# Performance work log

Measured on AMD Instinct MI355X. Metric: run time of the kernel, lower is better.

Reference implementation:

```python
import jax, jax.numpy as jnp
import numpy as np

N_DST = 25000
E = 400000
DN = 128   # dim_node
DE = 128   # dim_edge
DT = 128   # dim_time
DO = 128   # dim_out
H = 2      # num_head


def setup_inputs() -> dict:
    key = jax.random.key(0)
    ks = jax.random.split(key, 10)
    sc = 0.05
    node_h = jax.random.normal(ks[0], (N_DST + E, DN), jnp.float32)
    edge_f = jax.random.normal(ks[1], (E, DE), jnp.float32)
    dt = jax.random.uniform(ks[2], (E,), jnp.float32) * 100.0
    dst_idx = jax.random.randint(ks[3], (E,), 0, N_DST)
    # TimeEncode: Linear(1, dim_time) with w initialized to 1/10**linspace(0,9)
    time_w = jnp.asarray(1.0 / 10 ** np.linspace(0, 9, DT, dtype=np.float32))
    time_b = jnp.zeros((DT,), jnp.float32)
    Wq = jax.random.normal(ks[4], (DO, DN + DT), jnp.float32) * sc
    bq = jnp.zeros((DO,), jnp.float32)
    Wk = jax.random.normal(ks[5], (DO, DN + DE + DT), jnp.float32) * sc
    bk = jnp.zeros((DO,), jnp.float32)
    Wv = jax.random.normal(ks[6], (DO, DN + DE + DT), jnp.float32) * sc
    bv = jnp.zeros((DO,), jnp.float32)
    Wout = jax.random.normal(ks[7], (DO, DN + DO), jnp.float32) * sc
    bout = jnp.zeros((DO,), jnp.float32)
    gamma = jnp.ones((DO,), jnp.float32)
    beta = jnp.zeros((DO,), jnp.float32)
    return dict(node_h=node_h, edge_f=edge_f, dt=dt, dst_idx=dst_idx,
                time_w=time_w, time_b=time_b, Wq=Wq, bq=bq, Wk=Wk, bk=bk,
                Wv=Wv, bv=bv, Wout=Wout, bout=bout, gamma=gamma, beta=beta)


def reference(node_h, edge_f, dt, dst_idx, time_w, time_b,
              Wq, bq, Wk, bk, Wv, bv, Wout, bout, gamma, beta):
    num_dst = node_h.shape[0] - edge_f.shape[0]
    num_edges = edge_f.shape[0]
    tgt = node_h[:num_dst]            # [N, DN] target node embeddings
    src = node_h[num_dst:]            # [E, DN] per-edge source embeddings

    # TimeEncode: cos(w * dt + b)
    time_feats = jnp.cos(dt[:, None] * time_w[None, :] + time_b)          # [E, DT]
    zero_time = jnp.broadcast_to(jnp.cos(time_b), (num_dst, time_b.shape[0]))

    Qn = jnp.concatenate([tgt, zero_time], axis=1) @ Wq.T + bq            # [N, DO]
    kv_in = jnp.concatenate([src, edge_f, time_feats], axis=1)            # [E, DN+DE+DT]
    K = kv_in @ Wk.T + bk                                                 # [E, DO]
    V = kv_in @ Wv.T + bv                                                 # [E, DO]
    Q = Qn[dst_idx]                                                       # gather per edge

    d_head = Q.shape[1] // H
    Qh = Q.reshape(num_edges, H, d_head)
    Kh = K.reshape(num_edges, H, d_head)
    Vh = V.reshape(num_edges, H, d_head)

    score = jnp.sum(Qh * Kh, axis=2)                                      # [E, H]
    score = jnp.where(score >= 0, score, 0.2 * score)                     # LeakyReLU(0.2)

    # edge_softmax: segmented softmax over incoming edges of each dst node
    m = jax.ops.segment_max(score, dst_idx, num_segments=num_dst)
    m = jnp.where(jnp.isfinite(m), m, 0.0)                                # empty segments
    e = jnp.exp(score - m[dst_idx])
    s = jax.ops.segment_sum(e, dst_idx, num_segments=num_dst)
    att = e / s[dst_idx]                                                  # [E, H]

    Vw = (Vh * att[:, :, None]).reshape(num_edges, -1)                    # [E, DO]
    h = jax.ops.segment_sum(Vw, dst_idx, num_segments=num_dst)            # scatter-sum

    rst = jnp.concatenate([h, tgt], axis=1) @ Wout.T + bout               # [N, DO]
    rst = jax.nn.relu(rst)
    mu = jnp.mean(rst, axis=-1, keepdims=True)
    var = jnp.var(rst, axis=-1, keepdims=True)
    return (rst - mu) / jnp.sqrt(var + 1e-5) * gamma + beta
```

## Files before the change

kernel.cpp:

```cpp
#include <hip/hip_runtime.h>

#define N_DST 25000
#define E_NUM 400000

typedef __bf16 bf16x8 __attribute__((ext_vector_type(8)));
typedef __bf16 bf16x4 __attribute__((ext_vector_type(4)));
typedef __bf16 bf16x2 __attribute__((ext_vector_type(2)));
typedef float  f32x4  __attribute__((ext_vector_type(4)));

__device__ __forceinline__ float fast_cos(float x) {
  float r = x * 0.15915494309189535f;
  r = r - floorf(r);
  return __builtin_amdgcn_cosf(r);
}

__device__ __forceinline__ void pack_frag(const float* __restrict__ W0,
    const float* __restrict__ W1, int stride, int NC, int idx, __bf16* __restrict__ out) {
  int lane = idx & 63, fid = idx >> 6;
  int nfw = NC >> 6;
  int perks = nfw << 2;
  int ks = fid / perks, rem = fid - ks * perks;
  int w = rem / nfw, nf = rem - w * nfw;
  int n = w * (NC >> 2) + nf * 16 + (lane & 15);
  int g = (ks << 2) + (lane >> 4);
  const float* src = (W1 && n >= 128) ? (W1 + (size_t)(n - 128) * stride)
                                      : (W0 + (size_t)n * stride);
  const float4* s4 = reinterpret_cast<const float4*>(src + g * 8);
  float4 lo = s4[0], hi = s4[1];
  bf16x8 b;
  b[0]=(__bf16)lo.x; b[1]=(__bf16)lo.y; b[2]=(__bf16)lo.z; b[3]=(__bf16)lo.w;
  b[4]=(__bf16)hi.x; b[5]=(__bf16)hi.y; b[6]=(__bf16)hi.z; b[7]=(__bf16)hi.w;
  reinterpret_cast<bf16x8*>(out)[idx] = b;
}

__global__ __launch_bounds__(256) void prep_kernel(
    const float* __restrict__ Wq, const float* __restrict__ bq, const float* __restrict__ tb,
    const float* __restrict__ Wk, const float* __restrict__ Wv, const float* __restrict__ Wout,
    const int* __restrict__ dsti,
    float* __restrict__ cq, __bf16* __restrict__ Bq_kv, __bf16* __restrict__ Bq_q,
    __bf16* __restrict__ Bq_out, int* __restrict__ counts) {
  int b = blockIdx.x, tid = threadIdx.x;
  if (b == 0) {
    if (tid < 128) {
      float s = bq[tid];
      for (int j = 0; j < 128; ++j) s += cosf(tb[j]) * Wq[tid * 256 + 128 + j];
      cq[tid] = s;
    }
    return;
  }
  b -= 1;
  if (b < 48) { pack_frag(Wk, Wv, 384, 256, b * 256 + tid, Bq_kv); return; }
  b -= 48;
  if (b < 8)  { pack_frag(Wq, nullptr, 256, 128, b * 256 + tid, Bq_q); return; }
  b -= 8;
  if (b < 16) { pack_frag(Wout, nullptr, 256, 128, b * 256 + tid, Bq_out); return; }
  b -= 16;
  int e = b * 256 + tid;
  if (e < E_NUM) atomicAdd(&counts[dsti[e]], 1);
}

__global__ __launch_bounds__(1024) void scan_kernel(const int* __restrict__ counts,
    int* __restrict__ offs, int* __restrict__ cursor) {
  __shared__ int wpart[16];
  int tid = threadIdx.x, lane = tid & 63, wid = tid >> 6;
  int carry = 0;
  for (int base = 0; base < N_DST; base += 1024) {
    int idx = base + tid;
    int x = (idx < N_DST) ? counts[idx] : 0;
    int incl = x;
#pragma unroll
    for (int o = 1; o < 64; o <<= 1) {
      int y = __shfl_up(incl, o);
      if (lane >= o) incl += y;
    }
    if (lane == 63) wpart[wid] = incl;
    __syncthreads();
    if (wid == 0) {
      int v = (lane < 16) ? wpart[lane] : 0;
      int s = v;
#pragma unroll
      for (int o = 1; o < 16; o <<= 1) {
        int y = __shfl_up(s, o);
        if (lane >= o) s += y;
      }
      if (lane < 16) wpart[lane] = s;
    }
    __syncthreads();
    int woff = (wid > 0) ? wpart[wid - 1] : 0;
    int tot = wpart[15];
    if (idx < N_DST) {
      int v = carry + woff + incl - x;
      offs[idx] = v;
      cursor[idx] = v;
    }
    carry += tot;
    __syncthreads();
  }
  if (tid == 0) offs[N_DST] = carry;
}

__global__ __launch_bounds__(256) void fill_kernel(const int* __restrict__ dsti,
    int* __restrict__ cursor, int* __restrict__ elist, int* __restrict__ dsts) {
  int e = blockIdx.x * 256 + threadIdx.x;
  if (e < E_NUM) {
    int d = dsti[e];
    int p = atomicAdd(&cursor[d], 1);
    elist[p] = e;
    dsts[p] = d;
  }
}

template<int MODE>
__global__ __launch_bounds__(256, 4) void gemm_kernel(
    const float* __restrict__ A0, const float* __restrict__ A1,
    const float* __restrict__ dtp, const float* __restrict__ tw, const float* __restrict__ tb,
    const __bf16* __restrict__ Bq,
    const float* __restrict__ bias0, const float* __restrict__ bias1,
    const int* __restrict__ elist, const int* __restrict__ dsts,
    const float* __restrict__ Qn,
    float* __restrict__ outF, __bf16* __restrict__ Vout, float* __restrict__ score)
{
  constexpr int NC = (MODE == 1) ? 256 : 128;
  constexpr int NFRAGW = NC / 64;
  __shared__ __align__(16) char Abuf[2][64 * 256];
  __shared__ int Elds[64];
  __shared__ int Dlds[64];
  __shared__ float dts[64];
  __shared__ float twl[128];
  __shared__ float tbl[128];

  const int tid = threadIdx.x;
  const int e0 = blockIdx.x * 64;
  const int nv = (MODE == 1) ? 64 : min(64, N_DST - e0);
  const int srow = tid >> 5;
  const int sc4 = (tid & 31) << 2;

  const int lane = tid & 63;
  const int w = tid >> 6;
  const int nbase = w * (NC / 4);
  const int lrow = lane & 15;
  const int lk = lane >> 4;
  const int aswz = (lrow & 7) << 4;
  const bf16x8* __restrict__ Bw =
      reinterpret_cast<const bf16x8*>(Bq) + (size_t)(w * NFRAGW) * 64 + lane;

  f32x4 acc[4][NFRAGW];
#pragma unroll
  for (int mf = 0; mf < 4; ++mf)
#pragma unroll
    for (int nf = 0; nf < NFRAGW; ++nf)
      acc[mf][nf] = (f32x4){0.f, 0.f, 0.f, 0.f};

  auto issueA = [&](int t, float4 (&v)[8]) {
    if constexpr (MODE == 1) {
      const float* base = (t == 0) ? (A0 + (size_t)N_DST * 128) : A1;
#pragma unroll
      for (int i = 0; i < 8; ++i)
        v[i] = *reinterpret_cast<const float4*>(base + (size_t)Elds[srow + i * 8] * 128 + sc4);
    } else {
      const float* base = (t == 0) ? A0 : A1;
#pragma unroll
      for (int i = 0; i < 8; ++i) {
        int r = srow + i * 8;
        v[i] = (r < nv) ? *reinterpret_cast<const float4*>(base + (size_t)(e0 + r) * 128 + sc4)
                        : make_float4(0.f, 0.f, 0.f, 0.f);
      }
    }
  };
  auto writeA = [&](char* buf, float4 (&v)[8]) {
#pragma unroll
    for (int i = 0; i < 8; ++i) {
      int r = srow + i * 8;
      bf16x4 b;
      b[0]=(__bf16)v[i].x; b[1]=(__bf16)v[i].y; b[2]=(__bf16)v[i].z; b[3]=(__bf16)v[i].w;
      *reinterpret_cast<bf16x4*>(buf + r * 256 + ((sc4 * 2) ^ ((r & 7) << 4))) = b;
    }
  };
  auto cosW = [&](char* buf) {
    int r = tid >> 2;
    int j0 = (tid & 3) << 5;
    float d = dts[r];
    char* rowb = buf + r * 256;
    int swz = (r & 7) << 4;
#pragma unroll
    for (int i = 0; i < 16; ++i) {
      int j = j0 + i * 2;
      bf16x2 p;
      p[0] = (__bf16)fast_cos(d * twl[j] + tbl[j]);
      p[1] = (__bf16)fast_cos(d * twl[j + 1] + tbl[j + 1]);
      *reinterpret_cast<bf16x2*>(rowb + ((j * 2) ^ swz)) = p;
    }
  };
  auto ktile = [&](const char* buf, int t) {
#pragma unroll
    for (int ks = 0; ks < 4; ++ks) {
      bf16x8 b[NFRAGW];
#pragma unroll
      for (int nf = 0; nf < NFRAGW; ++nf)
        b[nf] = Bw[((size_t)(t * 4 + ks) * 4 * NFRAGW + nf) * 64];
      bf16x8 a[4];
#pragma unroll
      for (int mf = 0; mf < 4; ++mf)
        a[mf] = *reinterpret_cast<const bf16x8*>(
            buf + (mf * 16 + lrow) * 256 + (((ks * 32 + lk * 8) * 2) ^ aswz));
#pragma unroll
      for (int nf = 0; nf < NFRAGW; ++nf)
#pragma unroll
        for (int mf = 0; mf < 4; ++mf)
          acc[mf][nf] = __builtin_amdgcn_mfma_f32_16x16x32_bf16(a[mf], b[nf], acc[mf][nf], 0, 0, 0);
    }
  };

  if constexpr (MODE == 1) {
    if (tid < 64) {
      int e = elist[e0 + tid];
      Elds[tid] = e;
      Dlds[tid] = dsts[e0 + tid];
      dts[tid] = dtp[e];
    } else if (tid < 192) {
      int j = tid - 64;
      twl[j] = tw[j];
      tbl[j] = tb[j];
    }
    __syncthreads();
    float4 v[8];
    issueA(0, v);
    writeA(Abuf[0], v);
    __syncthreads();
    issueA(1, v);
    ktile(Abuf[0], 0);
    writeA(Abuf[1], v);
    __syncthreads();
    ktile(Abuf[1], 1);
    cosW(Abuf[0]);
    __syncthreads();
    ktile(Abuf[0], 2);
    __syncthreads();
    if (w >= 2) {
#pragma unroll
      for (int nf = 0; nf < NFRAGW; ++nf) {
        int vcol = (nbase - 128) + nf * 16 + lrow;
        float bb = bias1[vcol];
#pragma unroll
        for (int mf = 0; mf < 4; ++mf) {
#pragma unroll
          for (int r = 0; r < 4; ++r) {
            int row = mf * 16 + lk * 4 + r;
            *reinterpret_cast<__bf16*>(Abuf[0] + row * 256 + ((vcol * 2) ^ ((row & 7) << 4))) =
                (__bf16)(acc[mf][nf][r] + bb);
          }
        }
      }
    } else {
      float bkv[NFRAGW];
#pragma unroll
      for (int nf = 0; nf < NFRAGW; ++nf) bkv[nf] = bias0[nbase + nf * 16 + lrow];
#pragma unroll
      for (int mf = 0; mf < 4; ++mf) {
#pragma unroll
        for (int r = 0; r < 4; ++r) {
          int row = mf * 16 + lk * 4 + r;
          const float* qrow = Qn + ((size_t)Dlds[row] << 7) + w * 64;
          float s = 0.f;
#pragma unroll
          for (int nf = 0; nf < NFRAGW; ++nf)
            s += (acc[mf][nf][r] + bkv[nf]) * qrow[nf * 16 + lrow];
          s += __shfl_xor(s, 1);
          s += __shfl_xor(s, 2);
          s += __shfl_xor(s, 4);
          s += __shfl_xor(s, 8);
          if (lrow == 0) {
            s = (s >= 0.f) ? s : 0.2f * s;
            score[((size_t)(e0 + row) << 1) + w] = s;
          }
        }
      }
    }
    __syncthreads();
#pragma unroll
    for (int i = 0; i < 4; ++i) {
      int c = tid + i * 256;
      int r = c >> 4, cb = (c & 15) << 4;
      bf16x8 vv = *reinterpret_cast<const bf16x8*>(Abuf[0] + r * 256 + (cb ^ ((r & 7) << 4)));
      *reinterpret_cast<bf16x8*>(Vout + (((size_t)(e0 + r)) << 7) + (c & 15) * 8) = vv;
    }
  } else if constexpr (MODE == 0) {
    float4 v[8];
    issueA(0, v);
    writeA(Abuf[0], v);
    __syncthreads();
    ktile(Abuf[0], 0);
#pragma unroll
    for (int nf = 0; nf < NFRAGW; ++nf) {
      int col = nbase + nf * 16 + lrow;
      float bb = bias0[col];
#pragma unroll
      for (int mf = 0; mf < 4; ++mf) {
#pragma unroll
        for (int r = 0; r < 4; ++r) {
          int row = mf * 16 + lk * 4 + r;
          if (row < nv)
            outF[(size_t)(e0 + row) * 128 + col] = acc[mf][nf][r] + bb;
        }
      }
    }
  } else {
    float4 v[8];
    issueA(0, v);
    writeA(Abuf[0], v);
    __syncthreads();
    issueA(1, v);
    ktile(Abuf[0], 0);
    writeA(Abuf[1], v);
    __syncthreads();
    ktile(Abuf[1], 1);
    const float* gammaP = dtp;
    const float* betaP = tw;
    float vals[NFRAGW][4][4];
#pragma unroll
    for (int nf = 0; nf < NFRAGW; ++nf) {
      float bb = bias0[nbase + nf * 16 + lrow];
#pragma unroll
      for (int mf = 0; mf < 4; ++mf)
#pragma unroll
        for (int r = 0; r < 4; ++r)
          vals[nf][mf][r] = fmaxf(acc[mf][nf][r] + bb, 0.f);
    }
    __syncthreads();
    float* sums = reinterpret_cast<float*>(Abuf[0]);
    float* sqs  = reinterpret_cast<float*>(Abuf[0]) + 256;
    float* stats = reinterpret_cast<float*>(Abuf[0]) + 512;
#pragma unroll
    for (int mf = 0; mf < 4; ++mf) {
#pragma unroll
      for (int r = 0; r < 4; ++r) {
        float s1 = vals[0][mf][r] + vals[1][mf][r];
        float s2 = vals[0][mf][r] * vals[0][mf][r] + vals[1][mf][r] * vals[1][mf][r];
#pragma unroll
        for (int o = 1; o < 16; o <<= 1) {
          s1 += __shfl_xor(s1, o);
          s2 += __shfl_xor(s2, o);
        }
        if (lrow == 0) {
          int row = mf * 16 + lk * 4 + r;
          sums[w * 64 + row] = s1;
          sqs[w * 64 + row] = s2;
        }
      }
    }
    __syncthreads();
    if (tid < 64) {
      float s = sums[tid] + sums[64 + tid] + sums[128 + tid] + sums[192 + tid];
      float q = sqs[tid] + sqs[64 + tid] + sqs[128 + tid] + sqs[192 + tid];
      float mean = s * (1.f / 128.f);
      float var = q * (1.f / 128.f) - mean * mean;
      stats[tid * 2] = mean;
      stats[tid * 2 + 1] = rsqrtf(var + 1e-5f);
    }
    __syncthreads();
#pragma unroll
    for (int nf = 0; nf < NFRAGW; ++nf) {
      int col = nbase + nf * 16 + lrow;
      float g = gammaP[col], bC = betaP[col];
#pragma unroll
      for (int mf = 0; mf < 4; ++mf) {
#pragma unroll
        for (int r = 0; r < 4; ++r) {
          int row = mf * 16 + lk * 4 + r;
          if (row < nv) {
            float mean = stats[row * 2], rs = stats[row * 2 + 1];
            outF[(size_t)(e0 + row) * 128 + col] = (vals[nf][mf][r] - mean) * rs * g + bC;
          }
        }
      }
    }
  }
}

__global__ __launch_bounds__(256) void agg_kernel(const int* __restrict__ offs,
    const float* __restrict__ score, const __bf16* __restrict__ V, float* __restrict__ h) {
  int d = blockIdx.x * 4 + (threadIdx.x >> 6);
  if (d >= N_DST) return;
  int lane = threadIdx.x & 63;
  int beg = offs[d], end = offs[d + 1];
  int n = end - beg;
  float m0 = -3.0e38f, m1 = -3.0e38f;
  for (int i = lane; i < n; i += 64) {
    float2 sc = *reinterpret_cast<const float2*>(score + 2 * (size_t)(beg + i));
    m0 = fmaxf(m0, sc.x); m1 = fmaxf(m1, sc.y);
  }
#pragma unroll
  for (int o = 32; o; o >>= 1) {
    m0 = fmaxf(m0, __shfl_xor(m0, o));
    m1 = fmaxf(m1, __shfl_xor(m1, o));
  }
  float s0 = 0.f, s1 = 0.f;
  for (int i = lane; i < n; i += 64) {
    float2 sc = *reinterpret_cast<const float2*>(score + 2 * (size_t)(beg + i));
    s0 += __expf(sc.x - m0); s1 += __expf(sc.y - m1);
  }
#pragma unroll
  for (int o = 32; o; o >>= 1) {
    s0 += __shfl_xor(s0, o);
    s1 += __shfl_xor(s1, o);
  }
  float inv0 = (n > 0) ? 1.f / s0 : 0.f;
  float inv1 = (n > 0) ? 1.f / s1 : 0.f;
  int q = lane >> 4, j = lane & 15;
  int hsel = j >> 3;
  float acc[8];
#pragma unroll
  for (int k2 = 0; k2 < 8; ++k2) acc[k2] = 0.f;
  for (int i0 = 0; i0 < n; i0 += 4) {
    int i = i0 + q;
    if (i < n) {
      size_t p = beg + i;
      float2 sc = *reinterpret_cast<const float2*>(score + 2 * p);
      float wgt = hsel ? __expf(sc.y - m1) * inv1 : __expf(sc.x - m0) * inv0;
      bf16x8 v = *reinterpret_cast<const bf16x8*>(V + (p << 7) + j * 8);
#pragma unroll
      for (int k2 = 0; k2 < 8; ++k2) acc[k2] += wgt * (float)v[k2];
    }
  }
#pragma unroll
  for (int k2 = 0; k2 < 8; ++k2) {
    acc[k2] += __shfl_xor(acc[k2], 16);
    acc[k2] += __shfl_xor(acc[k2], 32);
  }
  if (q == 0) {
    float4 lo = make_float4(acc[0], acc[1], acc[2], acc[3]);
    float4 hi = make_float4(acc[4], acc[5], acc[6], acc[7]);
    float* dst = h + ((size_t)d << 7) + j * 8;
    *reinterpret_cast<float4*>(dst) = lo;
    *reinterpret_cast<float4*>(dst + 4) = hi;
  }
}

extern "C" void kernel_launch(void* const* d_in, const int* in_sizes, int n_in,
                              void* d_out, int out_size, void* d_ws, size_t ws_size,
                              hipStream_t stream) {
  (void)in_sizes; (void)n_in; (void)out_size; (void)ws_size;
  const float* node_h = (const float*)d_in[0];
  const float* edge_f = (const float*)d_in[1];
  const float* dtp    = (const float*)d_in[2];
  const int*   dsti   = (const int*)d_in[3];
  const float* tw     = (const float*)d_in[4];
  const float* tb     = (const float*)d_in[5];
  const float* Wq     = (const float*)d_in[6];
  const float* bq     = (const float*)d_in[7];
  const float* Wk     = (const float*)d_in[8];
  const float* bk     = (const float*)d_in[9];
  const float* Wv     = (const float*)d_in[10];
  const float* bv     = (const float*)d_in[11];
  const float* Wout   = (const float*)d_in[12];
  const float* bout   = (const float*)d_in[13];
  const float* gamma  = (const float*)d_in[14];
  const float* beta   = (const float*)d_in[15];
  float* outp = (float*)d_out;

  size_t off = 0;
  auto take = [&](size_t nbytes) -> void* {
    void* r = (char*)d_ws + off;
    off += (nbytes + 255) & ~(size_t)255;
    return r;
  };
  __bf16* Bq_kv  = (__bf16*)take((size_t)12288 * 16);
  __bf16* Bq_q   = (__bf16*)take((size_t)2048 * 16);
  __bf16* Bq_out = (__bf16*)take((size_t)4096 * 16);
  float*  cq     = (float*)take(128 * 4);
  float*  Qn     = (float*)take((size_t)N_DST * 128 * 4);
  __bf16* Vbuf   = (__bf16*)take((size_t)E_NUM * 128 * 2);
  float*  score  = (float*)take((size_t)E_NUM * 2 * 4);
  int*    counts = (int*)take((size_t)N_DST * 4);
  int*    offs   = (int*)take((size_t)(N_DST + 1) * 4);
  int*    cursor = (int*)take((size_t)N_DST * 4);
  int*    elist  = (int*)take((size_t)E_NUM * 4);
  int*    dsts   = (int*)take((size_t)E_NUM * 4);
  float*  hbuf   = (float*)take((size_t)N_DST * 128 * 4);

  hipMemsetAsync(counts, 0, (size_t)N_DST * 4, stream);

  const int count_blocks = (E_NUM + 255) / 256;
  prep_kernel<<<1 + 48 + 8 + 16 + count_blocks, 256, 0, stream>>>(
      Wq, bq, tb, Wk, Wv, Wout, dsti, cq, Bq_kv, Bq_q, Bq_out, counts);

  gemm_kernel<0><<<(N_DST + 63) / 64, 256, 0, stream>>>(node_h, nullptr, nullptr, nullptr, nullptr,
      Bq_q, cq, nullptr, nullptr, nullptr, nullptr, Qn, nullptr, nullptr);

  scan_kernel<<<1, 1024, 0, stream>>>(counts, offs, cursor);
  fill_kernel<<<count_blocks, 256, 0, stream>>>(dsti, cursor, elist, dsts);

  gemm_kernel<1><<<E_NUM / 64, 256, 0, stream>>>(node_h, edge_f, dtp, tw, tb,
      Bq_kv, bk, bv, elist, dsts, Qn, nullptr, Vbuf, score);

  agg_kernel<<<(N_DST + 3) / 4, 256, 0, stream>>>(offs, score, Vbuf, hbuf);

  gemm_kernel<2><<<(N_DST + 63) / 64, 256, 0, stream>>>(hbuf, node_h, gamma, beta, nullptr,
      Bq_out, bout, nullptr, nullptr, nullptr, nullptr, outp, nullptr, nullptr);
}
```

Baseline: 341.0 us.

## Split KV GEMM into dedicated kernel with async global-to-LDS fp32 staging

Moves the edge K/V projection out of the templated GEMM into a dedicated kernel. The A operand is staged as fp32 through direct global-to-LDS loads (global_load_lds), and the K dimension runs as six 64-wide tiles double-buffered so the next gather or cos tile is produced while the current one is multiplied. The bf16 conversion happens at fragment-load time from LDS. This aims to hide gather latency and drop the register round trip, at the cost of more LDS traffic, more conversion work and a sync every 64-K step.

```diff
diff --git a/kernel.cpp b/kernel.cpp
--- a/kernel.cpp
+++ b/kernel.cpp
@@ -12,6 +12,12 @@
   float r = x * 0.15915494309189535f;
   r = r - floorf(r);
   return __builtin_amdgcn_cosf(r);
+}
+
+__device__ __forceinline__ void gload_lds16(const void* g, void* l) {
+  __builtin_amdgcn_global_load_lds(
+      (const __attribute__((address_space(1))) unsigned int*)g,
+      (__attribute__((address_space(3))) unsigned int*)l, 16, 0, 0);
 }
 
 __device__ __forceinline__ void pack_frag(const float* __restrict__ W0,
@@ -110,19 +116,16 @@
   }
 }
 
-template<int MODE>
-__global__ __launch_bounds__(256, 4) void gemm_kernel(
-    const float* __restrict__ A0, const float* __restrict__ A1,
+__global__ __launch_bounds__(256, 4) void kv_kernel(
+    const float* __restrict__ node_h, const float* __restrict__ edge_f,
     const float* __restrict__ dtp, const float* __restrict__ tw, const float* __restrict__ tb,
     const __bf16* __restrict__ Bq,
-    const float* __restrict__ bias0, const float* __restrict__ bias1,
+    const float* __restrict__ bk, const float* __restrict__ bv,
     const int* __restrict__ elist, const int* __restrict__ dsts,
     const float* __restrict__ Qn,
-    float* __restrict__ outF, __bf16* __restrict__ Vout, float* __restrict__ score)
+    __bf16* __restrict__ Vout, float* __restrict__ score)
 {
-  constexpr int NC = (MODE == 1) ? 256 : 128;
-  constexpr int NFRAGW = NC / 64;
-  __shared__ __align__(16) char Abuf[2][64 * 256];
+  __shared__ __align__(16) float Abuf[2][4096];
   __shared__ int Elds[64];
   __shared__ int Dlds[64];
   __shared__ float dts[64];
@@ -131,7 +134,171 @@
 
   const int tid = threadIdx.x;
   const int e0 = blockIdx.x * 64;
-  const int nv = (MODE == 1) ? 64 : min(64, N_DST - e0);
+  const int lane = tid & 63;
+  const int w = tid >> 6;
+  const int lrow = lane & 15;
+  const int lk = lane >> 4;
+  const int aswz = (lrow & 7) << 4;
+
+  if (tid < 64) {
+    int e = elist[e0 + tid];
+    Elds[tid] = e;
+    Dlds[tid] = dsts[e0 + tid];
+    dts[tid] = dtp[e];
+  } else if (tid < 192) {
+    int j = tid - 64;
+    twl[j] = tw[j];
+    tbl[j] = tb[j];
+  }
+  __syncthreads();
+
+  auto stage_mem = [&](int t, int bufi) {
+    const float* base;
+    int coloff;
+    if (t < 2) { base = node_h + (size_t)N_DST * 128; coloff = t * 64; }
+    else       { base = edge_f;                       coloff = (t - 2) * 64; }
+#pragma unroll
+    for (int i = 0; i < 4; ++i) {
+      int g = w * 4 + i;
+      int r = g * 4 + (lane >> 4);
+      const float* src = base + (size_t)Elds[r] * 128 + coloff;
+      int boff = ((lane & 15) << 4) ^ ((r & 7) << 4);
+      gload_lds16((const char*)src + boff, &Abuf[bufi][g * 256]);
+    }
+  };
+  auto stage_cos = [&](int t, float* buf) {
+    int r = tid >> 2;
+    int j0 = (tid & 3) << 4;
+    float d = dts[r];
+    int swz = (r & 7) << 4;
+    char* rowb = (char*)(buf + r * 64);
+#pragma unroll
+    for (int q = 0; q < 4; ++q) {
+      f32x4 vv;
+#pragma unroll
+      for (int jj = 0; jj < 4; ++jj) {
+        int J = (t - 4) * 64 + j0 + q * 4 + jj;
+        vv[jj] = fast_cos(d * twl[J] + tbl[J]);
+      }
+      *reinterpret_cast<f32x4*>(rowb + (((j0 << 2) + (q << 4)) ^ swz)) = vv;
+    }
+  };
+
+  f32x4 acc[4][4];
+#pragma unroll
+  for (int mf = 0; mf < 4; ++mf)
+#pragma unroll
+    for (int nf = 0; nf < 4; ++nf)
+      acc[mf][nf] = (f32x4){0.f, 0.f, 0.f, 0.f};
+
+  const bf16x8* __restrict__ Bw = reinterpret_cast<const bf16x8*>(Bq) + (size_t)(w * 4) * 64 + lane;
+
+  auto ktile = [&](const float* buf, int t) {
+#pragma unroll
+    for (int ks = 0; ks < 2; ++ks) {
+      int K32 = t * 2 + ks;
+      bf16x8 b[4];
+#pragma unroll
+      for (int nf = 0; nf < 4; ++nf)
+        b[nf] = Bw[((size_t)K32 * 16 + nf) * 64];
+      bf16x8 a[4];
+#pragma unroll
+      for (int mf = 0; mf < 4; ++mf) {
+        const char* rowb = (const char*)(buf + (mf * 16 + lrow) * 64);
+        int cb = ks * 128 + lk * 32;
+        f32x4 f0 = *reinterpret_cast<const f32x4*>(rowb + (cb ^ aswz));
+        f32x4 f1 = *reinterpret_cast<const f32x4*>(rowb + ((cb + 16) ^ aswz));
+        bf16x8 av;
+#pragma unroll
+        for (int j = 0; j < 4; ++j) {
+          av[j] = (__bf16)f0[j];
+          av[4 + j] = (__bf16)f1[j];
+        }
+        a[mf] = av;
+      }
+#pragma unroll
+      for (int nf = 0; nf < 4; ++nf)
+#pragma unroll
+        for (int mf = 0; mf < 4; ++mf)
+          acc[mf][nf] = __builtin_amdgcn_mfma_f32_16x16x32_bf16(a[mf], b[nf], acc[mf][nf], 0, 0, 0);
+    }
+  };
+
+  stage_mem(0, 0);
+  __syncthreads();
+#pragma unroll
+  for (int t = 0; t < 6; ++t) {
+    if (t < 3) stage_mem(t + 1, (t + 1) & 1);
+    else if (t < 5) stage_cos(t + 1, Abuf[(t + 1) & 1]);
+    ktile(Abuf[t & 1], t);
+    __syncthreads();
+  }
+
+  char* Vlds = (char*)Abuf[0];
+  if (w >= 2) {
+#pragma unroll
+    for (int nf = 0; nf < 4; ++nf) {
+      int vcol = (w - 2) * 64 + nf * 16 + lrow;
+      float bb = bv[vcol];
+#pragma unroll
+      for (int mf = 0; mf < 4; ++mf) {
+#pragma unroll
+        for (int r = 0; r < 4; ++r) {
+          int row = mf * 16 + lk * 4 + r;
+          *reinterpret_cast<__bf16*>(Vlds + row * 256 + ((vcol * 2) ^ ((row & 7) << 4))) =
+              (__bf16)(acc[mf][nf][r] + bb);
+        }
+      }
+    }
+  } else {
+    float bkv[4];
+#pragma unroll
+    for (int nf = 0; nf < 4; ++nf) bkv[nf] = bk[w * 64 + nf * 16 + lrow];
+#pragma unroll
+    for (int mf = 0; mf < 4; ++mf) {
+#pragma unroll
+      for (int r = 0; r < 4; ++r) {
+        int row = mf * 16 + lk * 4 + r;
+        const float* qrow = Qn + ((size_t)Dlds[row] << 7) + w * 64;
+        float s = 0.f;
+#pragma unroll
+        for (int nf = 0; nf < 4; ++nf)
+          s += (acc[mf][nf][r] + bkv[nf]) * qrow[nf * 16 + lrow];
+        s += __shfl_xor(s, 1);
+        s += __shfl_xor(s, 2);
+        s += __shfl_xor(s, 4);
+        s += __shfl_xor(s, 8);
+        if (lrow == 0) {
+          s = (s >= 0.f) ? s : 0.2f * s;
+          score[((size_t)(e0 + row) << 1) + w] = s;
+        }
+      }
+    }
+  }
+  __syncthreads();
+#pragma unroll
+  for (int i = 0; i < 4; ++i) {
+    int c = tid + i * 256;
+    int r = c >> 4, cb = (c & 15) << 4;
+    bf16x8 vv = *reinterpret_cast<const bf16x8*>(Vlds + r * 256 + (cb ^ ((r & 7) << 4)));
+    *reinterpret_cast<bf16x8*>(Vout + (((size_t)(e0 + r)) << 7) + (c & 15) * 8) = vv;
+  }
+}
+
+template<int MODE>
+__global__ __launch_bounds__(256, 4) void gemm_kernel(
+    const float* __restrict__ A0, const float* __restrict__ A1,
+    const float* __restrict__ dtp, const float* __restrict__ tw,
+    const __bf16* __restrict__ Bq, const float* __restrict__ bias0,
+    float* __restrict__ outF)
+{
+  constexpr int NC = 128;
+  constexpr int NFRAGW = 2;
+  __shared__ __align__(16) char Abuf[2][64 * 256];
+
+  const int tid = threadIdx.x;
+  const int e0 = blockIdx.x * 64;
+  const int nv = min(64, N_DST - e0);
   const int srow = tid >> 5;
   const int sc4 = (tid & 31) << 2;
 
@@ -152,19 +319,12 @@
       acc[mf][nf] = (f32x4){0.f, 0.f, 0.f, 0.f};
 
   auto issueA = [&](int t, float4 (&v)[8]) {
-    if constexpr (MODE == 1) {
-      const float* base = (t == 0) ? (A0 + (size_t)N_DST * 128) : A1;
-#pragma unroll
-      for (int i = 0; i < 8; ++i)
-        v[i] = *reinterpret_cast<const float4*>(base + (size_t)Elds[srow + i * 8] * 128 + sc4);
-    } else {
-      const float* base = (t == 0) ? A0 : A1;
-#pragma unroll
-      for (int i = 0; i < 8; ++i) {
-        int r = srow + i * 8;
-        v[i] = (r < nv) ? *reinterpret_cast<const float4*>(base + (size_t)(e0 + r) * 128 + sc4)
-                        : make_float4(0.f, 0.f, 0.f, 0.f);
-      }
+    const float* base = (t == 0) ? A0 : A1;
+#pragma unroll
+    for (int i = 0; i < 8; ++i) {
+      int r = srow + i * 8;
+      v[i] = (r < nv) ? *reinterpret_cast<const float4*>(base + (size_t)(e0 + r) * 128 + sc4)
+                      : make_float4(0.f, 0.f, 0.f, 0.f);
     }
   };
   auto writeA = [&](char* buf, float4 (&v)[8]) {
@@ -176,21 +336,6 @@
       *reinterpret_cast<bf16x4*>(buf + r * 256 + ((sc4 * 2) ^ ((r & 7) << 4))) = b;
     }
   };
-  auto cosW = [&](char* buf) {
-    int r = tid >> 2;
-    int j0 = (tid & 3) << 5;
-    float d = dts[r];
-    char* rowb = buf + r * 256;
-    int swz = (r & 7) << 4;
-#pragma unroll
-    for (int i = 0; i < 16; ++i) {
-      int j = j0 + i * 2;
-      bf16x2 p;
-      p[0] = (__bf16)fast_cos(d * twl[j] + tbl[j]);
-      p[1] = (__bf16)fast_cos(d * twl[j + 1] + tbl[j + 1]);
-      *reinterpret_cast<bf16x2*>(rowb + ((j * 2) ^ swz)) = p;
-    }
-  };
   auto ktile = [&](const char* buf, int t) {
 #pragma unroll
     for (int ks = 0; ks < 4; ++ks) {
@@ -211,85 +356,21 @@
     }
   };
 
-  if constexpr (MODE == 1) {
-    if (tid < 64) {
-      int e = elist[e0 + tid];
-      Elds[tid] = e;
-      Dlds[tid] = dsts[e0 + tid];
-      dts[tid] = dtp[e];
-    } else if (tid < 192) {
-      int j = tid - 64;
-      twl[j] = tw[j];
-      tbl[j] = tb[j];
-    }
-    __syncthreads();
-    float4 v[8];
-    issueA(0, v);
-    writeA(Abuf[0], v);
-    __syncthreads();
+  float4 v[8];
+  issueA(0, v);
+  writeA(Abuf[0], v);
+  __syncthreads();
+  if constexpr (MODE == 2) {
     issueA(1, v);
     ktile(Abuf[0], 0);
     writeA(Abuf[1], v);
     __syncthreads();
     ktile(Abuf[1], 1);
-    cosW(Abuf[0]);
-    __syncthreads();
-    ktile(Abuf[0], 2);
-    __syncthreads();
-    if (w >= 2) {
-#pragma unroll
-      for (int nf = 0; nf < NFRAGW; ++nf) {
-        int vcol = (nbase - 128) + nf * 16 + lrow;
-        float bb = bias1[vcol];
-#pragma unroll
-        for (int mf = 0; mf < 4; ++mf) {
-#pragma unroll
-          for (int r = 0; r < 4; ++r) {
-            int row = mf * 16 + lk * 4 + r;
-            *reinterpret_cast<__bf16*>(Abuf[0] + row * 256 + ((vcol * 2) ^ ((row & 7) << 4))) =
-                (__bf16)(acc[mf][nf][r] + bb);
-          }
-        }
-      }
-    } else {
-      float bkv[NFRAGW];
-#pragma unroll
-      for (int nf = 0; nf < NFRAGW; ++nf) bkv[nf] = bias0[nbase + nf * 16 + lrow];
-#pragma unroll
-      for (int mf = 0; mf < 4; ++mf) {
-#pragma unroll
-        for (int r = 0; r < 4; ++r) {
-          int row = mf * 16 + lk * 4 + r;
-          const float* qrow = Qn + ((size_t)Dlds[row] << 7) + w * 64;
-          float s = 0.f;
-#pragma unroll
-          for (int nf = 0; nf < NFRAGW; ++nf)
-            s += (acc[mf][nf][r] + bkv[nf]) * qrow[nf * 16 + lrow];
-          s += __shfl_xor(s, 1);
-          s += __shfl_xor(s, 2);
-          s += __shfl_xor(s, 4);
-          s += __shfl_xor(s, 8);
-          if (lrow == 0) {
-            s = (s >= 0.f) ? s : 0.2f * s;
-            score[((size_t)(e0 + row) << 1) + w] = s;
-          }
-        }
-      }
-    }
-    __syncthreads();
-#pragma unroll
-    for (int i = 0; i < 4; ++i) {
-      int c = tid + i * 256;
-      int r = c >> 4, cb = (c & 15) << 4;
-      bf16x8 vv = *reinterpret_cast<const bf16x8*>(Abuf[0] + r * 256 + (cb ^ ((r & 7) << 4)));
-      *reinterpret_cast<bf16x8*>(Vout + (((size_t)(e0 + r)) << 7) + (c & 15) * 8) = vv;
-    }
-  } else if constexpr (MODE == 0) {
-    float4 v[8];
-    issueA(0, v);
-    writeA(Abuf[0], v);
-    __syncthreads();
+  } else {
     ktile(Abuf[0], 0);
+  }
+
+  if constexpr (MODE == 0) {
 #pragma unroll
     for (int nf = 0; nf < NFRAGW; ++nf) {
       int col = nbase + nf * 16 + lrow;
@@ -305,15 +386,6 @@
       }
     }
   } else {
-    float4 v[8];
-    issueA(0, v);
-    writeA(Abuf[0], v);
-    __syncthreads();
-    issueA(1, v);
-    ktile(Abuf[0], 0);
-    writeA(Abuf[1], v);
-    __syncthreads();
-    ktile(Abuf[1], 1);
     const float* gammaP = dtp;
     const float* betaP = tw;
     float vals[NFRAGW][4][4];
@@ -484,17 +556,17 @@
   prep_kernel<<<1 + 48 + 8 + 16 + count_blocks, 256, 0, stream>>>(
       Wq, bq, tb, Wk, Wv, Wout, dsti, cq, Bq_kv, Bq_q, Bq_out, counts);
 
-  gemm_kernel<0><<<(N_DST + 63) / 64, 256, 0, stream>>>(node_h, nullptr, nullptr, nullptr, nullptr,
-      Bq_q, cq, nullptr, nullptr, nullptr, nullptr, Qn, nullptr, nullptr);
+  gemm_kernel<0><<<(N_DST + 63) / 64, 256, 0, stream>>>(node_h, nullptr, nullptr, nullptr,
+      Bq_q, cq, Qn);
 
   scan_kernel<<<1, 1024, 0, stream>>>(counts, offs, cursor);
   fill_kernel<<<count_blocks, 256, 0, stream>>>(dsti, cursor, elist, dsts);
 
-  gemm_kernel<1><<<E_NUM / 64, 256, 0, stream>>>(node_h, edge_f, dtp, tw, tb,
-      Bq_kv, bk, bv, elist, dsts, Qn, nullptr, Vbuf, score);
+  kv_kernel<<<E_NUM / 64, 256, 0, stream>>>(node_h, edge_f, dtp, tw, tb,
+      Bq_kv, bk, bv, elist, dsts, Qn, Vbuf, score);
 
   agg_kernel<<<(N_DST + 3) / 4, 256, 0, stream>>>(offs, score, Vbuf, hbuf);
 
-  gemm_kernel<2><<<(N_DST + 63) / 64, 256, 0, stream>>>(hbuf, node_h, gamma, beta, nullptr,
-      Bq_out, bout, nullptr, nullptr, nullptr, nullptr, outp, nullptr, nullptr);
-}
+  gemm_kernel<2><<<(N_DST + 63) / 64, 256, 0, stream>>>(hbuf, node_h, gamma, beta,
+      Bq_out, bout, outp);
+}
```

After: 364.8 us. 7.0% more time.
